# Performance work log

Measured on AMD Instinct MI355X. Metric: run time of the kernel, lower is better.

The kernel has to match this reference:

```python
import jax, jax.numpy as jnp
import numpy as np
from jax import lax

K = 3
K2 = 9
PAD = 1
GN_GROUPS = 32
GN_EPS = 1e-5
COS_EPS = 1e-8


def conv2d(x, w):
    # 3x3, stride 1, pad 1, NCHW/OIHW
    return lax.conv_general_dilated(x, w, (1, 1), ((PAD, PAD), (PAD, PAD)),
                                    dimension_numbers=('NCHW', 'OIHW', 'NCHW'))


def group_norm(x, gamma, beta):
    N, C, H, W = x.shape
    xg = x.reshape(N, GN_GROUPS, C // GN_GROUPS, H, W)
    m = xg.mean(axis=(2, 3, 4), keepdims=True)
    v = xg.var(axis=(2, 3, 4), keepdims=True)
    xn = ((xg - m) * lax.rsqrt(v + GN_EPS)).reshape(N, C, H, W)
    return xn * gamma[None, :, None, None] + beta[None, :, None, None]


def deform_conv(x, offset, weight):
    # mmcv DeformConv, deformable_groups=1: offset [N, 2*K2, H, W] as (dy,dx) per kernel tap.
    N, C, H, W = x.shape
    off = offset.reshape(N, K2, 2, H, W)
    dy, dx = off[:, :, 0], off[:, :, 1]              # [N,K2,H,W]
    ky, kx = jnp.meshgrid(jnp.arange(K), jnp.arange(K), indexing='ij')
    ky = ky.reshape(K2).astype(x.dtype)
    kx = kx.reshape(K2).astype(x.dtype)
    hh = jnp.arange(H, dtype=x.dtype)
    ww = jnp.arange(W, dtype=x.dtype)
    # absolute (fractional) sample positions per output pixel and kernel tap
    py = hh[None, None, :, None] - PAD + ky[None, :, None, None] + dy   # [N,K2,H,W]
    px = ww[None, None, None, :] - PAD + kx[None, :, None, None] + dx
    y0 = jnp.floor(py)
    x0 = jnp.floor(px)
    ay = py - y0
    ax = px - x0
    xf = x.reshape(N, C, H * W)
    sampled = jnp.zeros((N, C, K2, H, W), x.dtype)
    for oy, wy in ((y0, 1.0 - ay), (y0 + 1.0, ay)):
        for ox, wx in ((x0, 1.0 - ax), (x0 + 1.0, ax)):
            valid = (oy >= 0) & (oy <= H - 1) & (ox >= 0) & (ox <= W - 1)
            yi = jnp.clip(oy, 0, H - 1).astype(jnp.int32)
            xi = jnp.clip(ox, 0, W - 1).astype(jnp.int32)
            idx = (yi * W + xi).reshape(N, 1, K2 * H * W)
            v = jnp.take_along_axis(xf, idx, axis=2).reshape(N, C, K2, H, W)
            w = jnp.where(valid, wy * wx, 0.0)[:, None]   # zero padding outside
            sampled = sampled + v * w
    O = weight.shape[0]
    return jnp.einsum('nckhw,ock->nohw', sampled, weight.reshape(O, C, K2))


def cos_sim(a, b):
    num = jnp.sum(a * b, axis=1)
    na = jnp.sqrt(jnp.sum(a * a, axis=1))
    nb = jnp.sqrt(jnp.sum(b * b, axis=1))
    return num / jnp.maximum(na * nb, COS_EPS)   # [N,H,W]


def agg(support, reference, layers):
    f = jnp.concatenate([support, reference], axis=1)
    for ow, ob, dw, gg, gb in layers[:3]:
        off = conv2d(f, ow) + ob[None, :, None, None]
        f = jax.nn.relu(group_norm(deform_conv(f, off, dw), gg, gb))
    ow, ob, dw, gg, gb = layers[3]
    off = conv2d(f, ow) + ob[None, :, None, None]
    return jax.nn.relu(group_norm(deform_conv(support, off, dw), gg, gb))


def setup_inputs() -> dict:
    key = jax.random.key(0)
    ks = jax.random.split(key, 16)
    C_in, C_out, H, W = 512, 256, 96, 96
    rn = lambda k, shape, s: jax.random.normal(k, shape, jnp.float32) * s
    inp = {'datas': jax.random.normal(ks[0], (2, C_out, H, W), jnp.float32)}
    i = 1
    for n in (1, 2, 3):
        inp[f'off{n}_w'] = rn(ks[i], (18, C_in, 3, 3), 0.01); i += 1
        inp[f'off{n}_b'] = jnp.zeros((18,), jnp.float32)
        inp[f'dcn{n}_w'] = rn(ks[i], (C_in, C_in, 3, 3), 0.02); i += 1
        inp[f'gn{n}_g'] = jnp.ones((C_in,), jnp.float32)
        inp[f'gn{n}_b'] = jnp.zeros((C_in,), jnp.float32)
    inp['off4_w'] = rn(ks[i], (18, C_in, 3, 3), 0.01); i += 1
    inp['off4_b'] = jnp.zeros((18,), jnp.float32)
    inp['dcn4_w'] = rn(ks[i], (C_out, C_out, 3, 3), 0.02); i += 1
    inp['gn4_g'] = jnp.ones((C_out,), jnp.float32)
    inp['gn4_b'] = jnp.zeros((C_out,), jnp.float32)
    return inp


def reference(datas, off1_w, off1_b, dcn1_w, gn1_g, gn1_b,
              off2_w, off2_b, dcn2_w, gn2_g, gn2_b,
              off3_w, off3_b, dcn3_w, gn3_g, gn3_b,
              off4_w, off4_b, dcn4_w, gn4_g, gn4_b):
    layers = [(off1_w, off1_b, dcn1_w, gn1_g, gn1_b),
              (off2_w, off2_b, dcn2_w, gn2_g, gn2_b),
              (off3_w, off3_b, dcn3_w, gn3_g, gn3_b),
              (off4_w, off4_b, dcn4_w, gn4_g, gn4_b)]
    support = datas[:1]
    reference_f = datas[1:]
    tt = agg(reference_f, reference_f, layers)   # [1,C_out,H,W]
    ttw = cos_sim(tt, tt)[:, None]               # [1,1,H,W]
    tk = agg(support, reference_f, layers)
    tkw = cos_sim(tt, tk)[:, None]
    w = jax.nn.softmax(jnp.stack([ttw, tkw], axis=0), axis=0)  # [2,1,1,H,W]
    f = jnp.stack([tt, tk], axis=0)                            # [2,1,C,H,W]
    return jnp.sum(w * f, axis=0)
```

## Files before the change

### kernel.cpp

```cpp
#include <hip/hip_runtime.h>
#include <math.h>

#define HW 9216
#define WIDTH 96
#define FSTRIDE (512*HW)
#define RSTRIDE (256*HW)
#define TABSTRIDE (9*HW)
#define PXP 12544
#define FTPROWS 12800

typedef __attribute__((ext_vector_type(8))) short bf16x8;
typedef __attribute__((ext_vector_type(4))) float f32x4;
typedef __attribute__((ext_vector_type(8))) unsigned short u16x8;

__device__ __forceinline__ unsigned short f2bf(float f) {
  unsigned int u = __float_as_uint(f);
  u += 0x7FFFu + ((u >> 16) & 1u);
  return (unsigned short)(u >> 16);
}
__device__ __forceinline__ float bf2f(unsigned short s) {
  return __uint_as_float(((unsigned int)s) << 16);
}

#define GLDS(g, l) __builtin_amdgcn_global_load_lds( \
    (const __attribute__((address_space(1))) unsigned int*)(g), \
    (__attribute__((address_space(3))) unsigned int*)(l), 16, 0, 0)

__global__ void k_zero(unsigned short* p, unsigned int n8) {
  unsigned int i = blockIdx.x * 256 + threadIdx.x;
  if (i < n8) ((u16x8*)p)[i] = (u16x8){0, 0, 0, 0, 0, 0, 0, 0};
}

__global__ void __launch_bounds__(256) k_mkftp_cat(
    const float* __restrict__ lo0, const float* __restrict__ lo1,
    const float* __restrict__ hi, unsigned short* __restrict__ dst,
    int C, int CB) {
  const int b = blockIdx.z;
  const float* lo = b ? lo1 : lo0;
  unsigned short* d = dst + (size_t)b * FTPROWS * C + 128 * C;
  const int px0 = blockIdx.x * 64, c0 = blockIdx.y * 64;
  __shared__ float tile[64][65];
  const int t = threadIdx.x;
#pragma unroll
  for (int rep = 0; rep < 16; ++rep) {
    int idx = rep * 256 + t;
    int cl = idx >> 6, pl = idx & 63;
    int cg = c0 + cl;
    const float* s = (cg < CB) ? (lo + (size_t)cg * HW) : (hi + (size_t)(cg - CB) * HW);
    tile[cl][pl] = s[px0 + pl];
  }
  __syncthreads();
  const int pl = t >> 2, cu = (t & 3) * 16;
  const int px = px0 + pl;
  const int h = px / WIDTH, w = px - h * WIDTH;
  const size_t pxp = (size_t)(h + 1) * 128 + (w + 1);
  u16x8 o0, o1;
#pragma unroll
  for (int j = 0; j < 8; ++j) o0[j] = f2bf(tile[cu + j][pl]);
#pragma unroll
  for (int j = 0; j < 8; ++j) o1[j] = f2bf(tile[cu + 8 + j][pl]);
  unsigned short* p = d + pxp * C + c0 + cu;
  *(u16x8*)p = o0;
  *(u16x8*)(p + 8) = o1;
}

__global__ void __launch_bounds__(256) k_mkftp_gn(
    const unsigned short* __restrict__ yh, const float2* __restrict__ stat,
    const float* __restrict__ gamma, const float* __restrict__ beta,
    unsigned short* __restrict__ dst) {
  const int C = 512;
  const int b = blockIdx.z;
  unsigned short* d = dst + (size_t)b * FTPROWS * C + 128 * C;
  const int px0 = blockIdx.x * 64, c0 = blockIdx.y * 64;
  __shared__ float tile[64][65];
  const int t = threadIdx.x;
#pragma unroll
  for (int rep = 0; rep < 16; ++rep) {
    int idx = rep * 256 + t;
    int cl = idx >> 6, pl = idx & 63;
    int cg = c0 + cl;
    float2 st = stat[b * 32 + (cg >> 4)];
    float v = bf2f(yh[(size_t)b * FSTRIDE + (size_t)cg * HW + px0 + pl]);
    v = (v - st.x) * st.y * gamma[cg] + beta[cg];
    tile[cl][pl] = fmaxf(v, 0.f);
  }
  __syncthreads();
  const int pl = t >> 2, cu = (t & 3) * 16;
  const int px = px0 + pl;
  const int h = px / WIDTH, w = px - h * WIDTH;
  const size_t pxp = (size_t)(h + 1) * 128 + (w + 1);
  u16x8 o0, o1;
#pragma unroll
  for (int j = 0; j < 8; ++j) o0[j] = f2bf(tile[cu + j][pl]);
#pragma unroll
  for (int j = 0; j < 8; ++j) o1[j] = f2bf(tile[cu + 8 + j][pl]);
  unsigned short* p = d + pxp * C + c0 + cu;
  *(u16x8*)p = o0;
  *(u16x8*)(p + 8) = o1;
}

__global__ void k_prepW(const float* __restrict__ ow, unsigned short* __restrict__ Wt) {
  int i = blockIdx.x * 256 + threadIdx.x;
  int k = i / (32 * 512), r = i - k * 32 * 512;
  int oc = r / 512, c = r - oc * 512;
  Wt[i] = (oc < 18) ? f2bf(ow[((size_t)oc * 512 + c) * 9 + k]) : (unsigned short)0;
}

__global__ void __launch_bounds__(256) k_offmm(const unsigned short* __restrict__ ftp,
                                               const unsigned short* __restrict__ Wt,
                                               float* __restrict__ part) {
  const int C = 512;
  __shared__ unsigned short As[2][128 * 64];
  __shared__ unsigned short Bs[2][32 * 64];
  const int tid = threadIdx.x;
  const int lane = tid & 63, wv = tid >> 6;
  const int b = blockIdx.z, ks = blockIdx.y;
  const int pxp0 = 128 + blockIdx.x * 128;
  const unsigned short* fb = ftp + (size_t)b * FTPROWS * C + 128 * C;

  const int lr = lane >> 3;
  const int lu = lane & 7;
  const int fr = lane & 15, hi = lane >> 4;

  f32x4 acc[2][2];
#pragma unroll
  for (int i = 0; i < 2; ++i)
#pragma unroll
    for (int j = 0; j < 2; ++j) acc[i][j] = (f32x4){0.f, 0.f, 0.f, 0.f};

#define OFFMM_STAGE(S, BUF)                                                   \
  {                                                                           \
    const int k_ = ks * 3 + ((S) >> 3);                                       \
    const int dlt_ = (k_ / 3 - 1) * 128 + (k_ % 3 - 1);                       \
    const int c0_ = ((S) & 7) * 64;                                           \
    _Pragma("unroll")                                                         \
    for (int q = 0; q < 4; ++q) {                                             \
      int row = wv * 32 + q * 8 + lr;                                         \
      int su = lu ^ (row & 7);                                                \
      GLDS(fb + (size_t)(pxp0 + dlt_ + row) * C + c0_ + su * 8,               \
           (char*)&As[BUF][0] + (wv * 32 + q * 8) * 128);                     \
    }                                                                         \
    {                                                                         \
      int row = wv * 8 + lr;                                                  \
      int su = lu ^ (row & 7);                                                \
      GLDS(Wt + ((size_t)k_ * 32 + row) * C + c0_ + su * 8,                   \
           (char*)&Bs[BUF][0] + wv * 8 * 128);                                \
    }                                                                         \
  }

  OFFMM_STAGE(0, 0);
  for (int s = 0; s < 24; ++s) {
    const int cur = s & 1;
    if (s + 1 < 24) {
      OFFMM_STAGE(s + 1, cur ^ 1);
      asm volatile("s_waitcnt vmcnt(5)" ::: "memory");
    } else {
      asm volatile("s_waitcnt vmcnt(0)" ::: "memory");
    }
    __builtin_amdgcn_s_barrier();
#pragma unroll
    for (int kk = 0; kk < 2; ++kk) {
      bf16x8 a[2], bb[2];
#pragma unroll
      for (int i = 0; i < 2; ++i) {
        int row = wv * 32 + i * 16 + fr;
        a[i] = *(const bf16x8*)&As[cur][row * 64 + (((kk * 4 + hi) ^ (row & 7)) * 8)];
      }
#pragma unroll
      for (int j = 0; j < 2; ++j) {
        int row = j * 16 + fr;
        bb[j] = *(const bf16x8*)&Bs[cur][row * 64 + (((kk * 4 + hi) ^ (row & 7)) * 8)];
      }
#pragma unroll
      for (int i = 0; i < 2; ++i)
#pragma unroll
        for (int j = 0; j < 2; ++j)
          acc[i][j] = __builtin_amdgcn_mfma_f32_16x16x32_bf16(a[i], bb[j], acc[i][j], 0, 0, 0);
    }
    __builtin_amdgcn_s_barrier();
  }

  float* pb = part + ((size_t)(b * 3 + ks)) * PXP * 32;
#pragma unroll
  for (int i = 0; i < 2; ++i)
#pragma unroll
    for (int j = 0; j < 2; ++j) {
      int row0 = pxp0 + wv * 32 + i * 16 + hi * 4;
      int col = j * 16 + fr;
#pragma unroll
      for (int q = 0; q < 4; ++q)
        pb[(size_t)(row0 + q) * 32 + col] = acc[i][j][q];
    }
}

__global__ void k_table(const float* __restrict__ part, const float* __restrict__ ob,
                        int4* __restrict__ tabi, float4* __restrict__ tabw) {
  int b = blockIdx.z, k = blockIdx.y;
  int px = blockIdx.x * 256 + threadIdx.x;
  int h = px / WIDTH, w = px - h * WIDTH;
  size_t pxp = (size_t)(h + 1) * 128 + (w + 1);
  const float* pb = part + (size_t)b * 3 * PXP * 32 + pxp * 32;
  float dy = ob[2 * k] + pb[2 * k] + pb[(size_t)PXP * 32 + 2 * k] + pb[2 * (size_t)PXP * 32 + 2 * k];
  float dx = ob[2 * k + 1] + pb[2 * k + 1] + pb[(size_t)PXP * 32 + 2 * k + 1] + pb[2 * (size_t)PXP * 32 + 2 * k + 1];
  float py = (float)(h - 1 + k / 3) + dy;
  float pxx = (float)(w - 1 + k % 3) + dx;
  float y0 = floorf(py), x0 = floorf(pxx);
  float ay = py - y0, ax = pxx - x0;
  float wy[2] = {1.f - ay, ay}, wx[2] = {1.f - ax, ax};
  int idx[4]; float wt[4];
#pragma unroll
  for (int t = 0; t < 4; ++t) {
    float oy = y0 + (float)(t >> 1);
    float ox = x0 + (float)(t & 1);
    bool valid = (oy >= 0.f) && (oy <= 95.f) && (ox >= 0.f) && (ox <= 95.f);
    int yi = (int)fminf(fmaxf(oy, 0.f), 95.f);
    int xi = (int)fminf(fmaxf(ox, 0.f), 95.f);
    idx[t] = (yi + 1) * 128 + (xi + 1);
    wt[t] = valid ? wy[t >> 1] * wx[t & 1] : 0.f;
  }
  size_t e = (size_t)b * TABSTRIDE + (size_t)k * HW + px;
  tabi[e] = make_int4(idx[0], idx[1], idx[2], idx[3]);
  tabw[e] = make_float4(wt[0], wt[1], wt[2], wt[3]);
}

__global__ void __launch_bounds__(256) k_sample_t(
    const unsigned short* __restrict__ ftp,
    const int4* __restrict__ tabi, const float4* __restrict__ tabw,
    unsigned short* __restrict__ samp, int C, int kbase, int rowK) {
  const int z = blockIdx.z;
  const int b = z & 1, kloc = z >> 1;
  const int k = kbase + kloc;
  const int t = threadIdx.x;
  const int px = blockIdx.x * 64 + (t >> 2);
  const int c = blockIdx.y * 64 + (t & 3) * 16;
  const unsigned short* fb = ftp + (size_t)b * FTPROWS * C + 128 * C;
  size_t e = (size_t)b * TABSTRIDE + (size_t)k * HW + px;
  int4 id = tabi[e];
  float4 wt = tabw[e];
  float acc[16];
#pragma unroll
  for (int j = 0; j < 16; ++j) acc[j] = 0.f;
  const int ids[4] = {id.x, id.y, id.z, id.w};
  const float wts[4] = {wt.x, wt.y, wt.z, wt.w};
#pragma unroll
  for (int s = 0; s < 4; ++s) {
    const unsigned short* p = fb + (size_t)ids[s] * C + c;
    u16x8 v0 = *(const u16x8*)p;
    u16x8 v1 = *(const u16x8*)(p + 8);
    float wgt = wts[s];
#pragma unroll
    for (int j = 0; j < 8; ++j) acc[j] += wgt * bf2f(v0[j]);
#pragma unroll
    for (int j = 0; j < 8; ++j) acc[8 + j] += wgt * bf2f(v1[j]);
  }
  u16x8 o0, o1;
#pragma unroll
  for (int j = 0; j < 8; ++j) o0[j] = f2bf(acc[j]);
#pragma unroll
  for (int j = 0; j < 8; ++j) o1[j] = f2bf(acc[8 + j]);
  unsigned short* dst = samp + ((size_t)b * HW + px) * rowK + kloc * C + c;
  *(u16x8*)dst = o0;
  *(u16x8*)(dst + 8) = o1;
}

__global__ void k_prepA(const float* __restrict__ dw, unsigned short* __restrict__ Ap,
                        int C) {
  int o = blockIdx.x * 256 + threadIdx.x;
  int K = 9 * C;
  int m = o / K, r = o - m * K;
  int k = r / C, c = r - k * C;
  Ap[o] = f2bf(dw[((size_t)m * C + c) * 9 + k]);
}

__device__ __forceinline__ void stage_ab96(const unsigned short* __restrict__ Ag,
                                           const unsigned short* __restrict__ Bg,
                                           int lda, int rowK, int kt,
                                           unsigned short* as_, unsigned short* bs_,
                                           int wv, int lane) {
  const int lr = lane >> 2;
  const int lu = lane & 3;
#pragma unroll
  for (int q = 0; q < 2; ++q) {
    int row = wv * 32 + q * 16 + lr;
    int su = lu ^ ((row >> 1) & 3);
    GLDS(Ag + (size_t)row * lda + kt + su * 8, (char*)as_ + (wv * 2 + q) * 1024);
  }
  const int nb = (wv < 2) ? 2 : 1;
  const int bu0 = (wv < 2) ? (2 * wv) : (wv + 2);
  for (int q = 0; q < nb; ++q) {
    int unit = bu0 + q;
    int row = unit * 16 + lr;
    int su = lu ^ ((row >> 1) & 3);
    GLDS(Bg + (size_t)row * rowK + kt + su * 8, (char*)bs_ + unit * 1024);
  }
}

__global__ void __launch_bounds__(256) k_dcgemm(
    const unsigned short* __restrict__ Ap, const unsigned short* __restrict__ Bt,
    unsigned short* __restrict__ Yh, float2* __restrict__ gnp,
    int lda, int rowK, int aOff, int accum, int CperG, int dogn) {
  __shared__ unsigned short As[3][128 * 32];
  __shared__ unsigned short Bs[3][96 * 32];
  const int tid = threadIdx.x;
  const int lane = tid & 63, wv = tid >> 6;

  const int nwg = gridDim.x;
  const int cpx = nwg >> 3;
  const int bid = blockIdx.x;
  const int l = (bid & 7) * cpx + (bid >> 3);
  const int nm = nwg / 192;
  const int m_i = l % nm;
  const int rest = l / nm;
  const int n_i = rest % 96;
  const int b = rest / 96;

  const int m0 = m_i << 7, n0 = n_i * 96;
  const unsigned short* Ag = Ap + (size_t)m0 * lda + aOff;
  const unsigned short* Bg = Bt + ((size_t)b * HW + n0) * rowK;

  const int wm = (wv >> 1) * 64, wn = (wv & 1) * 48;
  const int fr = lane & 15, hi = lane >> 4;
  const int nt = rowK >> 5;

  f32x4 acc[4][3];
#pragma unroll
  for (int i = 0; i < 4; ++i)
#pragma unroll
    for (int j = 0; j < 3; ++j) acc[i][j] = (f32x4){0.f, 0.f, 0.f, 0.f};

  stage_ab96(Ag, Bg, lda, rowK, 0,  &As[0][0], &Bs[0][0], wv, lane);
  stage_ab96(Ag, Bg, lda, rowK, 32, &As[1][0], &Bs[1][0], wv, lane);

  for (int t = 0; t < nt; ++t) {
    const int cur = t % 3;
    if (t + 2 < nt) {
      stage_ab96(Ag, Bg, lda, rowK, (t + 2) << 5, &As[(t + 2) % 3][0],
                 &Bs[(t + 2) % 3][0], wv, lane);
      if (wv < 2) asm volatile("s_waitcnt vmcnt(8)" ::: "memory");
      else        asm volatile("s_waitcnt vmcnt(6)" ::: "memory");
    } else if (t + 1 < nt) {
      if (wv < 2) asm volatile("s_waitcnt vmcnt(4)" ::: "memory");
      else        asm volatile("s_waitcnt vmcnt(3)" ::: "memory");
    } else {
      asm volatile("s_waitcnt vmcnt(0)" ::: "memory");
    }
    __builtin_amdgcn_s_barrier();
    __builtin_amdgcn_sched_barrier(0);
    bf16x8 a[4], bb[3];
#pragma unroll
    for (int i = 0; i < 4; ++i) {
      int row = wm + i * 16 + fr;
      a[i] = *(const bf16x8*)&As[cur][row * 32 + ((hi ^ ((row >> 1) & 3)) * 8)];
    }
#pragma unroll
    for (int j = 0; j < 3; ++j) {
      int row = wn + j * 16 + fr;
      bb[j] = *(const bf16x8*)&Bs[cur][row * 32 + ((hi ^ ((row >> 1) & 3)) * 8)];
    }
    __builtin_amdgcn_s_setprio(1);
#pragma unroll
    for (int i = 0; i < 4; ++i)
#pragma unroll
      for (int j = 0; j < 3; ++j)
        acc[i][j] = __builtin_amdgcn_mfma_f32_16x16x32_bf16(a[i], bb[j], acc[i][j], 0, 0, 0);
    __builtin_amdgcn_s_setprio(0);
    __builtin_amdgcn_s_barrier();
  }

  unsigned short* Yb = Yh + (size_t)b * FSTRIDE;
  const int orow = m0 + wm + hi * 4;
  const int ocol = n0 + wn + fr;
  float s_[4], q_[4];
#pragma unroll
  for (int i = 0; i < 4; ++i) { s_[i] = 0.f; q_[i] = 0.f; }
#pragma unroll
  for (int i = 0; i < 4; ++i) {
#pragma unroll
    for (int j = 0; j < 3; ++j) {
      unsigned short* p = Yb + (size_t)(orow + i * 16) * HW + ocol + j * 16;
#pragma unroll
      for (int q = 0; q < 4; ++q) {
        float v = acc[i][j][q];
        if (accum) v += bf2f(p[(size_t)q * HW]);
        p[(size_t)q * HW] = f2bf(v);
        s_[i] += v;
        q_[i] += v * v;
      }
    }
  }

  if (dogn) {
    const int redmax = (CperG == 16) ? 32 : 16;
#pragma unroll
    for (int i = 0; i < 4; ++i) {
      float s = s_[i], q = q_[i];
      for (int off = 1; off <= redmax; off <<= 1) {
        s += __shfl_xor(s, off);
        q += __shfl_xor(q, off);
      }
      int row0 = m0 + wm + i * 16 + ((CperG == 8) ? (lane >> 5) * 8 : 0);
      int g = row0 / CperG;
      bool writer = (CperG == 16) ? (lane == 0) : ((lane & 31) == 0);
      if (writer)
        gnp[(((size_t)(b * 32 + g)) * 96 + n_i) * 2 + (wv & 1)] = make_float2(s, q);
    }
  }
}

__global__ void k_gnfin2(const float2* __restrict__ gnp, float2* __restrict__ stat,
                         int CperG) {
  int t = threadIdx.x;
  float s = 0.f, q = 0.f;
  for (int j = 0; j < 192; ++j) {
    float2 v = gnp[(size_t)t * 192 + j];
    s += v.x; q += v.y;
  }
  float n = (float)(CperG * HW);
  float m = s / n;
  float var = q / n - m * m;
  stat[t] = make_float2(m, rsqrtf(var + 1e-5f));
}

__global__ void __launch_bounds__(256) k_gnstats1h(const unsigned short* __restrict__ yh,
                                                   float2* __restrict__ part, int CperG) {
  const int b = blockIdx.z, g = blockIdx.x, ch = blockIdx.y;
  const int n = CperG * HW;
  const int cs8 = (n >> 4) >> 3;
  const u16x8* p = (const u16x8*)(yh + (size_t)b * FSTRIDE + (size_t)g * n + (size_t)ch * (n >> 4));
  float s = 0.f, q = 0.f;
  for (int i = threadIdx.x; i < cs8; i += 256) {
    u16x8 v = p[i];
#pragma unroll
    for (int j = 0; j < 8; ++j) { float f = bf2f(v[j]); s += f; q += f * f; }
  }
  __shared__ float ss[256], qs[256];
  ss[threadIdx.x] = s; qs[threadIdx.x] = q;
  __syncthreads();
  for (int d = 128; d > 0; d >>= 1) {
    if (threadIdx.x < d) { ss[threadIdx.x] += ss[threadIdx.x + d]; qs[threadIdx.x] += qs[threadIdx.x + d]; }
    __syncthreads();
  }
  if (threadIdx.x == 0) part[((b << 5) + g) * 16 + ch] = make_float2(ss[0], qs[0]);
}

__global__ void k_gnfin(const float2* __restrict__ part, float2* __restrict__ stat,
                        int CperG) {
  int t = threadIdx.x;
  float s = 0.f, q = 0.f;
#pragma unroll
  for (int j = 0; j < 16; ++j) { float2 v = part[t * 16 + j]; s += v.x; q += v.y; }
  float n = (float)(CperG * HW);
  float m = s / n;
  float var = q / n - m * m;
  stat[t] = make_float2(m, rsqrtf(var + 1e-5f));
}

__global__ void k_gnapply(const unsigned short* __restrict__ yh,
                          const float2* __restrict__ stat,
                          const float* __restrict__ gamma, const float* __restrict__ beta,
                          float* __restrict__ out, int CperG, size_t ostride) {
  int b = blockIdx.z;
  int i = (blockIdx.x * 256 + threadIdx.x) * 4;
  int c = i / HW;
  float2 st = stat[b * 32 + c / CperG];
  float ga = gamma[c], be = beta[c];
  ushort4 vv = *(const ushort4*)(yh + (size_t)b * FSTRIDE + i);
  float4 v = make_float4(bf2f(vv.x), bf2f(vv.y), bf2f(vv.z), bf2f(vv.w));
  v.x = fmaxf((v.x - st.x) * st.y * ga + be, 0.f);
  v.y = fmaxf((v.y - st.x) * st.y * ga + be, 0.f);
  v.z = fmaxf((v.z - st.x) * st.y * ga + be, 0.f);
  v.w = fmaxf((v.w - st.x) * st.y * ga + be, 0.f);
  *(float4*)(out + (size_t)b * ostride + i) = v;
}

__global__ void k_cos1(const float* __restrict__ res, float4* __restrict__ part) {
  int px = blockIdx.x * 256 + threadIdx.x;
  int cc = blockIdx.y;
  float saa = 0.f, sbb = 0.f, sab = 0.f;
  for (int c = cc * 32; c < cc * 32 + 32; ++c) {
    float a = res[(size_t)c * HW + px];
    float bb = res[(size_t)RSTRIDE + (size_t)c * HW + px];
    saa += a * a; sbb += bb * bb; sab += a * bb;
  }
  part[(size_t)cc * HW + px] = make_float4(saa, sbb, sab, 0.f);
}

__global__ void k_cos2(const float4* __restrict__ part, float* __restrict__ wpix) {
  int px = blockIdx.x * 256 + threadIdx.x;
  float saa = 0.f, sbb = 0.f, sab = 0.f;
#pragma unroll
  for (int cc = 0; cc < 8; ++cc) {
    float4 v = part[(size_t)cc * HW + px];
    saa += v.x; sbb += v.y; sab += v.z;
  }
  float na = sqrtf(saa), nb = sqrtf(sbb);
  float ttw = saa / fmaxf(na * na, 1e-8f);
  float tkw = sab / fmaxf(na * nb, 1e-8f);
  float m = fmaxf(ttw, tkw);
  float e0 = expf(ttw - m), e1 = expf(tkw - m);
  wpix[px] = e0 / (e0 + e1);
}

__global__ void k_combine(const float* __restrict__ res, const float* __restrict__ wpix,
                          float* __restrict__ out) {
  int i = blockIdx.x * 256 + threadIdx.x;
  int px = i % HW;
  float w0 = wpix[px];
  out[i] = w0 * res[i] + (1.f - w0) * res[(size_t)RSTRIDE + i];
}

extern "C" void kernel_launch(void* const* d_in, const int* in_sizes, int n_in,
                              void* d_out, int out_size, void* d_ws, size_t ws_size,
                              hipStream_t stream) {
  const float* datas = (const float*)d_in[0];
  const float* ow[4] = {(const float*)d_in[1], (const float*)d_in[6],
                        (const float*)d_in[11], (const float*)d_in[16]};
  const float* ob[4] = {(const float*)d_in[2], (const float*)d_in[7],
                        (const float*)d_in[12], (const float*)d_in[17]};
  const float* dw[4] = {(const float*)d_in[3], (const float*)d_in[8],
                        (const float*)d_in[13], (const float*)d_in[18]};
  const float* gg[4] = {(const float*)d_in[4], (const float*)d_in[9],
                        (const float*)d_in[14], (const float*)d_in[19]};
  const float* gb[4] = {(const float*)d_in[5], (const float*)d_in[10],
                        (const float*)d_in[15], (const float*)d_in[20]};

  const int fullk = (ws_size >= 236400000ull) ? 1 : 0;
  const size_t sampN = fullk ? (2 * (size_t)HW * 4608) : (2 * (size_t)HW * 1536);

  float* ws = (float*)d_ws;
  unsigned short* yh = (unsigned short*)ws;
  float* offp3 = ws + (2 * (size_t)FSTRIDE * 2) / 4;
  float4* tabw = (float4*)(offp3 + 2 * 3 * (size_t)PXP * 32);
  int4*   tabi = (int4*)(tabw + 2 * (size_t)TABSTRIDE);
  float* wpix = (float*)(tabi + 2 * (size_t)TABSTRIDE);
  float2* stat = (float2*)(wpix + HW);
  float2* gnp  = stat + 64;
  float2* gnpart = gnp + 2 * 32 * 96 * 2;
  float4* cospart = (float4*)(gnpart + 1024);
  float* endp = (float*)(cospart + 8 * (size_t)HW);
  size_t ofs = ((size_t)(endp - ws) + 3) & ~(size_t)3;
  unsigned short* samp = (unsigned short*)(ws + ofs);
  unsigned short* Ap = samp + sampN;
  unsigned short* Wt = Ap + (size_t)512 * 4608;
  unsigned short* ftp512 = Wt + (size_t)9 * 32 * 512;
  unsigned short* ftp256 = fullk ? (samp + 2 * (size_t)HW * 2304)
                                 : (ftp512 + 2 * (size_t)FTPROWS * 512);
  float* res = (float*)(ftp256 + 2 * (size_t)FTPROWS * 256);

  dim3 blk(256);
  k_zero<<<dim3(2 * FTPROWS * 512 / 8 / 256), blk, 0, stream>>>(ftp512, 2u * FTPROWS * 512 / 8);

  for (int lyr = 0; lyr < 4; ++lyr) {
    const int Cx = (lyr < 3) ? 512 : 256;
    const int M  = Cx;
    const int CperG = (lyr < 3) ? 16 : 8;
    if (lyr == 0) {
      k_mkftp_cat<<<dim3(144, 8, 2), blk, 0, stream>>>(datas + RSTRIDE, datas,
                                                       datas + RSTRIDE, ftp512, 512, 256);
    } else {
      k_mkftp_gn<<<dim3(144, 8, 2), blk, 0, stream>>>(yh, stat, gg[lyr - 1], gb[lyr - 1],
                                                      ftp512);
    }
    k_prepA<<<dim3(M * 9 * Cx / 256), blk, 0, stream>>>(dw[lyr], Ap, Cx);
    k_prepW<<<dim3(9 * 32 * 512 / 256), blk, 0, stream>>>(ow[lyr], Wt);
    k_offmm<<<dim3(96, 3, 2), blk, 0, stream>>>(ftp512, Wt, offp3);
    k_table<<<dim3(36, 9, 2), blk, 0, stream>>>(offp3, ob[lyr], tabi, tabw);
    const unsigned short* sftp;
    if (lyr < 3) {
      sftp = ftp512;
    } else {
      k_zero<<<dim3(2 * FTPROWS * 256 / 8 / 256), blk, 0, stream>>>(ftp256, 2u * FTPROWS * 256 / 8);
      k_mkftp_cat<<<dim3(144, 4, 2), blk, 0, stream>>>(datas + RSTRIDE, datas,
                                                       datas, ftp256, 256, 256);
      sftp = ftp256;
    }
    const int nch = fullk ? 1 : 3;
    const int nk = 9 / nch;
    const int rowK = nk * Cx;
    for (int ch = 0; ch < nch; ++ch) {
      k_sample_t<<<dim3(144, Cx / 64, 2 * nk), blk, 0, stream>>>(sftp, tabi, tabw, samp,
                                                                 Cx, ch * nk, rowK);
      k_dcgemm<<<dim3((M / 128) * 96 * 2), blk, 0, stream>>>(
          Ap, samp, yh, gnp, 9 * Cx, rowK, ch * rowK, ch > 0, CperG,
          fullk && (ch == nch - 1));
    }
    if (fullk) {
      k_gnfin2<<<dim3(1), dim3(64), 0, stream>>>(gnp, stat, CperG);
    } else {
      k_gnstats1h<<<dim3(32, 16, 2), blk, 0, stream>>>(yh, gnpart, CperG);
      k_gnfin<<<dim3(1), dim3(64), 0, stream>>>(gnpart, stat, CperG);
    }
  }

  k_gnapply<<<dim3(RSTRIDE / 1024, 1, 2), blk, 0, stream>>>(yh, stat, gg[3], gb[3], res,
                                                            8, (size_t)RSTRIDE);
  k_cos1<<<dim3(36, 8), blk, 0, stream>>>(res, cospart);
  k_cos2<<<dim3(36), blk, 0, stream>>>(cospart, wpix);
  k_combine<<<dim3(RSTRIDE / 256), blk, 0, stream>>>(res, wpix, (float*)d_out);
}
```

Before: 978.4 us.

## Use two waves per GEMM block with 64x96 per-wave tiles

The deformable-conv GEMM block drops from 4 waves to 2, so each wave now computes a 64x96 output sub-tile (4x6 MFMA fragments) instead of 64x48. Global-to-LDS staging, waitcnt thresholds and the group-norm partial-sum layout (one partial per column tile instead of two) are adjusted to match, and the finalize kernel reads 96 partials. The aim is more MFMA work per LDS fragment load and fewer barriers per block. The cost is fewer waves available to hide latency, which may hurt latency hiding and occupancy, plus higher register pressure from 24 accumulators.

```diff
diff --git a/kernel.cpp b/kernel.cpp
--- a/kernel.cpp
+++ b/kernel.cpp
@@ -272,30 +272,28 @@
   Ap[o] = f2bf(dw[((size_t)m * C + c) * 9 + k]);
 }
 
-__device__ __forceinline__ void stage_ab96(const unsigned short* __restrict__ Ag,
-                                           const unsigned short* __restrict__ Bg,
-                                           int lda, int rowK, int kt,
-                                           unsigned short* as_, unsigned short* bs_,
-                                           int wv, int lane) {
+__device__ __forceinline__ void stage_ab96w2(const unsigned short* __restrict__ Ag,
+                                             const unsigned short* __restrict__ Bg,
+                                             int lda, int rowK, int kt,
+                                             unsigned short* as_, unsigned short* bs_,
+                                             int wv, int lane) {
   const int lr = lane >> 2;
   const int lu = lane & 3;
 #pragma unroll
-  for (int q = 0; q < 2; ++q) {
-    int row = wv * 32 + q * 16 + lr;
+  for (int q = 0; q < 4; ++q) {
+    int row = wv * 64 + q * 16 + lr;
     int su = lu ^ ((row >> 1) & 3);
-    GLDS(Ag + (size_t)row * lda + kt + su * 8, (char*)as_ + (wv * 2 + q) * 1024);
-  }
-  const int nb = (wv < 2) ? 2 : 1;
-  const int bu0 = (wv < 2) ? (2 * wv) : (wv + 2);
-  for (int q = 0; q < nb; ++q) {
-    int unit = bu0 + q;
-    int row = unit * 16 + lr;
+    GLDS(Ag + (size_t)row * lda + kt + su * 8, (char*)as_ + (wv * 4 + q) * 1024);
+  }
+#pragma unroll
+  for (int q = 0; q < 3; ++q) {
+    int row = wv * 48 + q * 16 + lr;
     int su = lu ^ ((row >> 1) & 3);
-    GLDS(Bg + (size_t)row * rowK + kt + su * 8, (char*)bs_ + unit * 1024);
-  }
-}
-
-__global__ void __launch_bounds__(256) k_dcgemm(
+    GLDS(Bg + (size_t)row * rowK + kt + su * 8, (char*)bs_ + (wv * 3 + q) * 1024);
+  }
+}
+
+__global__ void __launch_bounds__(128) k_dcgemm(
     const unsigned short* __restrict__ Ap, const unsigned short* __restrict__ Bt,
     unsigned short* __restrict__ Yh, float2* __restrict__ gnp,
     int lda, int rowK, int aOff, int accum, int CperG, int dogn) {
@@ -318,50 +316,48 @@
   const unsigned short* Ag = Ap + (size_t)m0 * lda + aOff;
   const unsigned short* Bg = Bt + ((size_t)b * HW + n0) * rowK;
 
-  const int wm = (wv >> 1) * 64, wn = (wv & 1) * 48;
+  const int wm = wv * 64;
   const int fr = lane & 15, hi = lane >> 4;
   const int nt = rowK >> 5;
 
-  f32x4 acc[4][3];
+  f32x4 acc[4][6];
 #pragma unroll
   for (int i = 0; i < 4; ++i)
 #pragma unroll
-    for (int j = 0; j < 3; ++j) acc[i][j] = (f32x4){0.f, 0.f, 0.f, 0.f};
-
-  stage_ab96(Ag, Bg, lda, rowK, 0,  &As[0][0], &Bs[0][0], wv, lane);
-  stage_ab96(Ag, Bg, lda, rowK, 32, &As[1][0], &Bs[1][0], wv, lane);
+    for (int j = 0; j < 6; ++j) acc[i][j] = (f32x4){0.f, 0.f, 0.f, 0.f};
+
+  stage_ab96w2(Ag, Bg, lda, rowK, 0,  &As[0][0], &Bs[0][0], wv, lane);
+  stage_ab96w2(Ag, Bg, lda, rowK, 32, &As[1][0], &Bs[1][0], wv, lane);
 
   for (int t = 0; t < nt; ++t) {
     const int cur = t % 3;
     if (t + 2 < nt) {
-      stage_ab96(Ag, Bg, lda, rowK, (t + 2) << 5, &As[(t + 2) % 3][0],
-                 &Bs[(t + 2) % 3][0], wv, lane);
-      if (wv < 2) asm volatile("s_waitcnt vmcnt(8)" ::: "memory");
-      else        asm volatile("s_waitcnt vmcnt(6)" ::: "memory");
+      stage_ab96w2(Ag, Bg, lda, rowK, (t + 2) << 5, &As[(t + 2) % 3][0],
+                   &Bs[(t + 2) % 3][0], wv, lane);
+      asm volatile("s_waitcnt vmcnt(14)" ::: "memory");
     } else if (t + 1 < nt) {
-      if (wv < 2) asm volatile("s_waitcnt vmcnt(4)" ::: "memory");
-      else        asm volatile("s_waitcnt vmcnt(3)" ::: "memory");
+      asm volatile("s_waitcnt vmcnt(7)" ::: "memory");
     } else {
       asm volatile("s_waitcnt vmcnt(0)" ::: "memory");
     }
     __builtin_amdgcn_s_barrier();
     __builtin_amdgcn_sched_barrier(0);
-    bf16x8 a[4], bb[3];
+    bf16x8 a[4], bb[6];
 #pragma unroll
     for (int i = 0; i < 4; ++i) {
       int row = wm + i * 16 + fr;
       a[i] = *(const bf16x8*)&As[cur][row * 32 + ((hi ^ ((row >> 1) & 3)) * 8)];
     }
 #pragma unroll
-    for (int j = 0; j < 3; ++j) {
-      int row = wn + j * 16 + fr;
+    for (int j = 0; j < 6; ++j) {
+      int row = j * 16 + fr;
       bb[j] = *(const bf16x8*)&Bs[cur][row * 32 + ((hi ^ ((row >> 1) & 3)) * 8)];
     }
     __builtin_amdgcn_s_setprio(1);
 #pragma unroll
     for (int i = 0; i < 4; ++i)
 #pragma unroll
-      for (int j = 0; j < 3; ++j)
+      for (int j = 0; j < 6; ++j)
         acc[i][j] = __builtin_amdgcn_mfma_f32_16x16x32_bf16(a[i], bb[j], acc[i][j], 0, 0, 0);
     __builtin_amdgcn_s_setprio(0);
     __builtin_amdgcn_s_barrier();
@@ -369,14 +365,14 @@
 
   unsigned short* Yb = Yh + (size_t)b * FSTRIDE;
   const int orow = m0 + wm + hi * 4;
-  const int ocol = n0 + wn + fr;
+  const int ocol = n0 + fr;
   float s_[4], q_[4];
 #pragma unroll
   for (int i = 0; i < 4; ++i) { s_[i] = 0.f; q_[i] = 0.f; }
 #pragma unroll
   for (int i = 0; i < 4; ++i) {
 #pragma unroll
-    for (int j = 0; j < 3; ++j) {
+    for (int j = 0; j < 6; ++j) {
       unsigned short* p = Yb + (size_t)(orow + i * 16) * HW + ocol + j * 16;
 #pragma unroll
       for (int q = 0; q < 4; ++q) {
@@ -402,7 +398,7 @@
       int g = row0 / CperG;
       bool writer = (CperG == 16) ? (lane == 0) : ((lane & 31) == 0);
       if (writer)
-        gnp[(((size_t)(b * 32 + g)) * 96 + n_i) * 2 + (wv & 1)] = make_float2(s, q);
+        gnp[((size_t)(b * 32 + g)) * 96 + n_i] = make_float2(s, q);
     }
   }
 }
@@ -411,8 +407,8 @@
                          int CperG) {
   int t = threadIdx.x;
   float s = 0.f, q = 0.f;
-  for (int j = 0; j < 192; ++j) {
-    float2 v = gnp[(size_t)t * 192 + j];
+  for (int j = 0; j < 96; ++j) {
+    float2 v = gnp[(size_t)t * 96 + j];
     s += v.x; q += v.y;
   }
   float n = (float)(CperG * HW);
@@ -580,7 +576,7 @@
     for (int ch = 0; ch < nch; ++ch) {
       k_sample_t<<<dim3(144, Cx / 64, 2 * nk), blk, 0, stream>>>(sftp, tabi, tabw, samp,
                                                                  Cx, ch * nk, rowK);
-      k_dcgemm<<<dim3((M / 128) * 96 * 2), blk, 0, stream>>>(
+      k_dcgemm<<<dim3((M / 128) * 96 * 2), dim3(128), 0, stream>>>(
           Ap, samp, yh, gnp, 9 * Cx, rowK, ch * rowK, ch > 0, CperG,
           fullk && (ch == nch - 1));
     }
```

After: 1.216 ms. 1.24x slower.
